# Optimization experiments

Hardware: AMD Instinct MI355X
Metric: run time of the kernel (lower is better)

## Reference

```python
import jax, jax.numpy as jnp
import numpy as np

N_NODES = 100000
N_EDGES = 1600000
IN_NODE = 129
HID = 128
N_LAYERS = 3


def setup_inputs() -> dict:
    key = jax.random.key(0)
    ks = jax.random.split(key, 20)
    gnn_in = IN_NODE - 1
    x = jax.random.normal(ks[0], (N_NODES, IN_NODE), dtype=jnp.float32)
    edge_index = jax.random.randint(ks[1], (2, N_EDGES), 0, N_NODES, dtype=jnp.int64)
    edge_attr = jax.random.uniform(ks[2], (N_EDGES, 1), dtype=jnp.float32)
    # conv layer params: lin (in->hid) per layer, scalar edge mlp per layer
    dims = [gnn_in] + [HID] * N_LAYERS
    conv_W, conv_b, edge_w = [], [], []
    for i in range(N_LAYERS):
        fin = dims[i]
        s = 1.0 / np.sqrt(fin)
        conv_W.append(jax.random.uniform(ks[3 + i], (fin, HID), jnp.float32, -s, s))
        conv_b.append(jax.random.uniform(ks[6 + i], (HID,), jnp.float32, -s, s))
        edge_w.append(jax.random.uniform(ks[9 + i], (1, 1), jnp.float32, -1.0, 1.0))
    h2 = HID // 2
    t_h = IN_NODE // 2
    s1 = 1.0 / np.sqrt(HID + 1)
    s2 = 1.0 / np.sqrt(h2)
    s3 = 1.0 / np.sqrt(IN_NODE)
    s4 = 1.0 / np.sqrt(t_h)
    return {
        "x": x, "edge_index": edge_index, "edge_attr": edge_attr,
        "conv_W": tuple(conv_W), "conv_b": tuple(conv_b), "edge_w": tuple(edge_w),
        "lin1_W": jax.random.uniform(ks[12], (HID + 1, h2), jnp.float32, -s1, s1),
        "lin1_b": jax.random.uniform(ks[13], (h2,), jnp.float32, -s1, s1),
        "lin2_W": jax.random.uniform(ks[14], (h2, 1), jnp.float32, -s2, s2),
        "lin2_b": jax.random.uniform(ks[15], (1,), jnp.float32, -s2, s2),
        "t1_W": jax.random.uniform(ks[16], (IN_NODE, t_h), jnp.float32, -s3, s3),
        "t1_b": jax.random.uniform(ks[17], (t_h,), jnp.float32, -s3, s3),
        "t2_W": jax.random.uniform(ks[18], (t_h, 1), jnp.float32, -s4, s4),
        "t2_b": jax.random.uniform(ks[19], (1,), jnp.float32, -s4, s4),
    }


def reference(x, edge_index, edge_attr, conv_W, conv_b, edge_w,
              lin1_W, lin1_b, lin2_W, lin2_b, t1_W, t1_b, t2_W, t2_b):
    n = x.shape[0]
    # add self loops with edge_attr fill_value = 1.0
    loops = jnp.arange(n, dtype=edge_index.dtype)
    src = jnp.concatenate([edge_index[0], loops])
    tgt = jnp.concatenate([edge_index[1], loops])
    ea = jnp.concatenate([edge_attr, jnp.ones((n, 1), edge_attr.dtype)], axis=0)  # [E+N,1]
    # in-degree for mean aggregation (>=1 because of self loops)
    deg = jax.ops.segment_sum(jnp.ones_like(ea[:, 0]), tgt, num_segments=n)[:, None]
    # treatment head (eval mode: no dropout)
    t = jax.nn.relu(x @ t1_W + t1_b)
    t = jax.nn.sigmoid(t @ t2_W + t2_b)  # [N,1]
    h = x[:, 1:]
    for W, b, w in zip(conv_W, conv_b, edge_w):
        ht = h @ W + b                          # [N,HID]
        gate = jax.nn.sigmoid(ea * w[0, 0])     # [E+N,1]
        msg = gate * ht[src]                    # gather + gate
        agg = jax.ops.segment_sum(msg, tgt, num_segments=n) / deg
        h = jax.nn.relu(agg)
    z = jnp.concatenate([h, t], axis=1)          # [N,HID+1]
    z = jax.nn.relu(z @ lin1_W + lin1_b)
    out = jax.nn.sigmoid(z @ lin2_W + lin2_b)[:, 0]  # [N]
    return out
```

## Files before the change

kernel.cpp:

```cpp
#include <hip/hip_runtime.h>
#include <hip/hip_fp16.h>
#include <math.h>


typedef _Float16 f16x8 __attribute__((ext_vector_type(8)));
typedef float f32x4 __attribute__((ext_vector_type(4)));

#define EPB 1024

__device__ __forceinline__ float sigmoidf_(float v) { return 1.f / (1.f + expf(-v)); }

__global__ void sentinel_kernel(float* __restrict__ out, int n, float val) {
  int i = blockIdx.x * 256 + threadIdx.x;
  if (i < n) out[i] = val;
}

__global__ void flag_kernel(const int* __restrict__ ei, int* __restrict__ flag) {
  if (threadIdx.x == 0 && blockIdx.x == 0) {
    int all0 = 1;
    for (int k = 1; k < 512; k += 2) {
      if (ei[k] != 0) { all0 = 0; break; }
    }
    *flag = all0;
  }
}

__global__ __launch_bounds__(256) void hist_kernel(const int* __restrict__ ei,
    int E, int n, const int* __restrict__ flag, int* __restrict__ histA,
    int nblocksA, int NB) {
  __shared__ int hl[512];
  for (int i = threadIdx.x; i < NB; i += 256) hl[i] = 0;
  __syncthreads();
  int f64 = *flag;
  const long long* e64 = (const long long*)ei;
  int base = blockIdx.x * EPB;
  int end = min(base + EPB, E);
  for (int e = base + threadIdx.x; e < end; e += 256) {
    int t = f64 ? (int)e64[(size_t)E + e] : ei[(size_t)E + e];
    if ((unsigned)t < (unsigned)n) atomicAdd(&hl[t >> 8], 1);
  }
  __syncthreads();
  for (int i = threadIdx.x; i < NB; i += 256)
    histA[(size_t)i * nblocksA + blockIdx.x] = hl[i];
}

__global__ __launch_bounds__(256) void scanrow_kernel(int* __restrict__ histA,
    int nblocksA, int* __restrict__ binTotal) {
  __shared__ int tmp[256];
  int bin = blockIdx.x;
  int* row = histA + (size_t)bin * nblocksA;
  int carry = 0;
  for (int c0 = 0; c0 < nblocksA; c0 += 256) {
    int i = c0 + threadIdx.x;
    int v = (i < nblocksA) ? row[i] : 0;
    tmp[threadIdx.x] = v;
    __syncthreads();
    for (int off = 1; off < 256; off <<= 1) {
      int t = (threadIdx.x >= (unsigned)off) ? tmp[threadIdx.x - off] : 0;
      __syncthreads();
      tmp[threadIdx.x] += t;
      __syncthreads();
    }
    if (i < nblocksA) row[i] = carry + tmp[threadIdx.x] - v;
    carry += tmp[255];
    __syncthreads();
  }
  if (threadIdx.x == 0) binTotal[bin] = carry;
}

__global__ void binbase_kernel(const int* __restrict__ binTotal, int NB,
                               int* __restrict__ binBase, int* __restrict__ starts,
                               int n) {
  __shared__ int tmp[512];
  int v = (threadIdx.x < (unsigned)NB) ? binTotal[threadIdx.x] : 0;
  tmp[threadIdx.x] = v;
  __syncthreads();
  for (int off = 1; off < 512; off <<= 1) {
    int t = (threadIdx.x >= (unsigned)off) ? tmp[threadIdx.x - off] : 0;
    __syncthreads();
    tmp[threadIdx.x] += t;
    __syncthreads();
  }
  if (threadIdx.x < (unsigned)NB) binBase[threadIdx.x] = tmp[threadIdx.x] - v;
  if (threadIdx.x == (unsigned)(NB - 1)) {
    binBase[NB] = tmp[threadIdx.x];
    starts[n] = tmp[threadIdx.x];
  }
}

__global__ __launch_bounds__(256) void reorder_kernel(const int* __restrict__ ei,
    const float* __restrict__ ea, int E, int n, const int* __restrict__ flag,
    const int* __restrict__ histA, int nblocksA, const int* __restrict__ binBase,
    const float* __restrict__ w0p, const float* __restrict__ w1p,
    const float* __restrict__ w2p, uint2* __restrict__ brec,
    unsigned char* __restrict__ bkey, int NB) {
  __shared__ int cur[512];
  for (int i = threadIdx.x; i < NB; i += 256)
    cur[i] = binBase[i] + histA[(size_t)i * nblocksA + blockIdx.x];
  __syncthreads();
  float w0 = w0p[0], w1 = w1p[0], w2 = w2p[0];
  int f64 = *flag;
  const long long* e64 = (const long long*)ei;
  int base = blockIdx.x * EPB;
  int end = min(base + EPB, E);
  for (int e = base + threadIdx.x; e < end; e += 256) {
    int s, t;
    if (f64) { s = (int)e64[e]; t = (int)e64[(size_t)E + e]; }
    else     { s = ei[e];       t = ei[(size_t)E + e]; }
    if ((unsigned)t < (unsigned)n) {
      int pos = atomicAdd(&cur[t >> 8], 1);
      float a = ea[e];
      unsigned sn = (unsigned)min(max(s, 0), min(n - 1, 0x1ffff));
      unsigned g0 = (unsigned)__float2uint_rn(sigmoidf_(a * w0) * 32767.f);
      unsigned g1 = (unsigned)__float2uint_rn(sigmoidf_(a * w1) * 32767.f);
      unsigned g2 = (unsigned)__float2uint_rn(sigmoidf_(a * w2) * 32767.f);
      brec[pos] = make_uint2(sn | (g0 << 17), g1 | (g2 << 15));
      bkey[pos] = (unsigned char)(t & 255);
    }
  }
}

__global__ __launch_bounds__(256) void fine_kernel(const uint2* __restrict__ brec,
    const unsigned char* __restrict__ bkey, const int* __restrict__ binBase,
    int n, uint2* __restrict__ csr, int* __restrict__ starts) {
  __shared__ int cnt[256];
  __shared__ int offs[256];
  __shared__ int tmp[256];
  int bin = blockIdx.x;
  int b0 = binBase[bin], b1 = binBase[bin + 1];
  cnt[threadIdx.x] = 0;
  __syncthreads();
  for (int p = b0 + threadIdx.x; p < b1; p += 256)
    atomicAdd(&cnt[bkey[p]], 1);
  __syncthreads();
  int v = cnt[threadIdx.x];
  tmp[threadIdx.x] = v;
  __syncthreads();
  for (int off = 1; off < 256; off <<= 1) {
    int t = (threadIdx.x >= (unsigned)off) ? tmp[threadIdx.x - off] : 0;
    __syncthreads();
    tmp[threadIdx.x] += t;
    __syncthreads();
  }
  offs[threadIdx.x] = tmp[threadIdx.x] - v;
  int node = bin * 256 + threadIdx.x;
  if (node < n) starts[node] = b0 + offs[threadIdx.x];
  __syncthreads();
  cnt[threadIdx.x] = 0;
  __syncthreads();
  for (int p = b0 + threadIdx.x; p < b1; p += 256) {
    int k = bkey[p];
    int l = atomicAdd(&cnt[k], 1);
    csr[b0 + offs[k] + l] = brec[p];
  }
}

__global__ void slice_kernel(const float* __restrict__ x, _Float16* __restrict__ h,
                             float* __restrict__ x0, int n) {
  int idx = blockIdx.x * blockDim.x + threadIdx.x;
  if (idx < n * 128) {
    int node = idx >> 7;
    int k = idx & 127;
    h[idx] = (_Float16)x[(size_t)node * 129 + 1 + k];
  }
  if (idx < n) x0[idx] = x[(size_t)idx * 129];
}

__global__ __launch_bounds__(256) void head_mfma_kernel(const _Float16* __restrict__ h,
    const float* __restrict__ extra, const float* __restrict__ W1,
    const float* __restrict__ b1, const float* __restrict__ w2,
    const float* __restrict__ b2, float* __restrict__ out, int n,
    int hrow0, int xrow) {
  __shared__ __align__(16) _Float16 sB[4 * 4 * 64 * 8];
  __shared__ float sWx[64], sB1[64], sW2[64];
  for (int idx = threadIdx.x; idx < 8192; idx += 256) {
    int k = idx >> 6, col = idx & 63;
    float w = W1[(size_t)(hrow0 + k) * 64 + col];
    int ks = k >> 5, quad = (k >> 3) & 3, j = k & 7;
    int nt = col >> 4, cl = col & 15;
    sB[(((ks * 4 + nt) * 64) + quad * 16 + cl) * 8 + j] = (_Float16)w;
  }
  if (threadIdx.x < 64) {
    sWx[threadIdx.x] = W1[(size_t)xrow * 64 + threadIdx.x];
    sB1[threadIdx.x] = b1[threadIdx.x];
    sW2[threadIdx.x] = w2[threadIdx.x];
  }
  __syncthreads();
  int wv = threadIdx.x >> 6, lane = threadIdx.x & 63;
  int quad = lane >> 4, l15 = lane & 15;
  int n0 = (blockIdx.x * 4 + wv) * 16;
  if (n0 >= n) return;
  int node_a = min(n0 + l15, n - 1);
  const _Float16* hrow = h + (size_t)node_a * 128 + quad * 8;

  f32x4 acc[4];
#pragma unroll
  for (int t = 0; t < 4; t++) acc[t] = (f32x4){0.f, 0.f, 0.f, 0.f};
  for (int ks = 0; ks < 4; ks++) {
    f16x8 afrag = *(const f16x8*)(hrow + ks * 32);
    const f16x8* bp = (const f16x8*)sB;
#pragma unroll
    for (int t = 0; t < 4; t++) {
      f16x8 bfrag = bp[(ks * 4 + t) * 64 + lane];
      acc[t] = __builtin_amdgcn_mfma_f32_16x16x32_f16(afrag, bfrag, acc[t], 0, 0, 0);
    }
  }
  float b2v = b2[0];
  float xv[4], part[4] = {0.f, 0.f, 0.f, 0.f};
#pragma unroll
  for (int r = 0; r < 4; r++) xv[r] = extra[min(n0 + quad * 4 + r, n - 1)];
#pragma unroll
  for (int t = 0; t < 4; t++) {
    int col = t * 16 + l15;
    float wx = sWx[col], bb = sB1[col], w2v = sW2[col];
#pragma unroll
    for (int r = 0; r < 4; r++) {
      float u = fmaxf(acc[t][r] + xv[r] * wx + bb, 0.f);
      part[r] += u * w2v;
    }
  }
#pragma unroll
  for (int r = 0; r < 4; r++) {
    float p = part[r];
    p += __shfl_xor(p, 1); p += __shfl_xor(p, 2);
    p += __shfl_xor(p, 4); p += __shfl_xor(p, 8);
    int node = n0 + quad * 4 + r;
    if (l15 == 0 && node < n) out[node] = sigmoidf_(p + b2v);
  }
}

__global__ __launch_bounds__(256) void gemm_mfma_kernel(const _Float16* __restrict__ h,
    const float* __restrict__ Wg, const float* __restrict__ b,
    unsigned char* __restrict__ out8, float* __restrict__ scales, int n) {
  __shared__ __align__(16) _Float16 sB[4 * 8 * 64 * 8];
  for (int i = threadIdx.x; i < 4096; i += 256) {
    int k = i >> 5;
    int n4 = (i & 31) * 4;
    float4 w4 = ((const float4*)Wg)[i];
    int ks = k >> 5, quad = (k >> 3) & 3, j = k & 7;
#pragma unroll
    for (int c = 0; c < 4; c++) {
      int col = n4 + c;
      int nt = col >> 4, cl = col & 15;
      sB[(((ks * 8 + nt) * 64) + quad * 16 + cl) * 8 + j] =
          (_Float16)((const float*)&w4)[c];
    }
  }
  __syncthreads();
  int wv = threadIdx.x >> 6, lane = threadIdx.x & 63;
  int quad = lane >> 4, l15 = lane & 15;
  int tiles = (n + 63) >> 6;
  for (int tile = blockIdx.x; tile < tiles; tile += gridDim.x) {
    int n0 = (tile * 4 + wv) * 16;
    if (n0 >= n) continue;
    int node_a = min(n0 + l15, n - 1);
    const _Float16* hrow = h + (size_t)node_a * 128 + quad * 8;

    f32x4 acc[8];
#pragma unroll
    for (int t = 0; t < 8; t++) acc[t] = (f32x4){0.f, 0.f, 0.f, 0.f};

    for (int ks = 0; ks < 4; ks++) {
      f16x8 afrag = *(const f16x8*)(hrow + ks * 32);
      const f16x8* bp = (const f16x8*)(sB + ks * 8 * 64 * 8);
#pragma unroll
      for (int t = 0; t < 8; t++) {
        f16x8 bfrag = bp[t * 64 + lane];
        acc[t] = __builtin_amdgcn_mfma_f32_16x16x32_f16(afrag, bfrag, acc[t], 0, 0, 0);
      }
    }
#pragma unroll
    for (int t = 0; t < 8; t++) {
      float bias = b[t * 16 + l15];
#pragma unroll
      for (int r = 0; r < 4; r++) acc[t][r] += bias;
    }
    float mx[4] = {0.f, 0.f, 0.f, 0.f};
#pragma unroll
    for (int t = 0; t < 8; t++)
#pragma unroll
      for (int r = 0; r < 4; r++) mx[r] = fmaxf(mx[r], fabsf(acc[t][r]));
#pragma unroll
    for (int m = 1; m <= 8; m <<= 1) {
#pragma unroll
      for (int r = 0; r < 4; r++) mx[r] = fmaxf(mx[r], __shfl_xor(mx[r], m));
    }
#pragma unroll
    for (int r = 0; r < 4; r++) {
      int node = n0 + quad * 4 + r;
      if (node >= n) continue;
      float inv = (mx[r] > 0.f) ? 127.f / mx[r] : 0.f;
      if (l15 == 0) scales[node] = mx[r] * (1.f / 127.f);
#pragma unroll
      for (int t = 0; t < 8; t++) {
        int u = (int)rintf(acc[t][r] * inv) + 128;
        u = min(max(u, 0), 255);
        out8[(size_t)node * 128 + t * 16 + l15] = (unsigned char)u;
      }
    }
  }
}

template <int LAYER>
__device__ __forceinline__ float gate_(uint2 r) {
  const float inv = 1.f / 32767.f;
  if (LAYER == 0) return (float)(r.x >> 17) * inv;
  if (LAYER == 1) return (float)(r.y & 0x7fffu) * inv;
  return (float)(r.y >> 15) * inv;
}

#define ACC4(u, g)                                   \
  a0 += (float)((u) & 0xffu) * (g);                  \
  a1 += (float)(((u) >> 8) & 0xffu) * (g);           \
  a2 += (float)(((u) >> 16) & 0xffu) * (g);          \
  a3 += (float)((u) >> 24) * (g);

template <int LAYER>
__global__ __launch_bounds__(256) void agg_kernel(const unsigned char* __restrict__ ht8,
    const float* __restrict__ scales, const uint2* __restrict__ csr,
    const int* __restrict__ starts, const float* __restrict__ wp,
    __half2* __restrict__ hout, int n) {
  int wv = threadIdx.x >> 6, lane = threadIdx.x & 63;
  int node = blockIdx.x * 4 + wv;
  if (node >= n) return;
  int s = starts[node];
  int c = starts[node + 1] - s;
  float gs = sigmoidf_(wp[0]);
  int sub = lane & 31, p = lane >> 5;
  unsigned sub4 = (unsigned)sub * 4u;

  unsigned su = *(const unsigned*)(ht8 + (unsigned)node * 128u + sub4);
  float gsc = (p == 0) ? gs * scales[node] : 0.f;
  float sgs = gsc;
  float a0 = 0.f, a1 = 0.f, a2 = 0.f, a3 = 0.f;
  ACC4(su, gsc)

  int j = 0;
  for (; j + 16 <= c; j += 16) {
    uint2 r0 = csr[s + j + 0 + p],  r1 = csr[s + j + 2 + p];
    uint2 r2 = csr[s + j + 4 + p],  r3 = csr[s + j + 6 + p];
    uint2 r4 = csr[s + j + 8 + p],  r5 = csr[s + j + 10 + p];
    uint2 r6 = csr[s + j + 12 + p], r7 = csr[s + j + 14 + p];
    unsigned i0 = r0.x & 0x1ffffu, i1 = r1.x & 0x1ffffu;
    unsigned i2 = r2.x & 0x1ffffu, i3 = r3.x & 0x1ffffu;
    unsigned i4 = r4.x & 0x1ffffu, i5 = r5.x & 0x1ffffu;
    unsigned i6 = r6.x & 0x1ffffu, i7 = r7.x & 0x1ffffu;
    unsigned u0 = *(const unsigned*)(ht8 + i0 * 128u + sub4);
    unsigned u1 = *(const unsigned*)(ht8 + i1 * 128u + sub4);
    unsigned u2 = *(const unsigned*)(ht8 + i2 * 128u + sub4);
    unsigned u3 = *(const unsigned*)(ht8 + i3 * 128u + sub4);
    unsigned u4 = *(const unsigned*)(ht8 + i4 * 128u + sub4);
    unsigned u5 = *(const unsigned*)(ht8 + i5 * 128u + sub4);
    unsigned u6 = *(const unsigned*)(ht8 + i6 * 128u + sub4);
    unsigned u7 = *(const unsigned*)(ht8 + i7 * 128u + sub4);
    float g0 = gate_<LAYER>(r0) * scales[i0];
    float g1 = gate_<LAYER>(r1) * scales[i1];
    float g2 = gate_<LAYER>(r2) * scales[i2];
    float g3 = gate_<LAYER>(r3) * scales[i3];
    float g4 = gate_<LAYER>(r4) * scales[i4];
    float g5 = gate_<LAYER>(r5) * scales[i5];
    float g6 = gate_<LAYER>(r6) * scales[i6];
    float g7 = gate_<LAYER>(r7) * scales[i7];
    sgs += g0 + g1 + g2 + g3 + g4 + g5 + g6 + g7;
    ACC4(u0, g0) ACC4(u1, g1) ACC4(u2, g2) ACC4(u3, g3)
    ACC4(u4, g4) ACC4(u5, g5) ACC4(u6, g6) ACC4(u7, g7)
  }
  for (; j + 8 <= c; j += 8) {
    uint2 r0 = csr[s + j + 0 + p], r1 = csr[s + j + 2 + p];
    uint2 r2 = csr[s + j + 4 + p], r3 = csr[s + j + 6 + p];
    unsigned i0 = r0.x & 0x1ffffu, i1 = r1.x & 0x1ffffu;
    unsigned i2 = r2.x & 0x1ffffu, i3 = r3.x & 0x1ffffu;
    unsigned u0 = *(const unsigned*)(ht8 + i0 * 128u + sub4);
    unsigned u1 = *(const unsigned*)(ht8 + i1 * 128u + sub4);
    unsigned u2 = *(const unsigned*)(ht8 + i2 * 128u + sub4);
    unsigned u3 = *(const unsigned*)(ht8 + i3 * 128u + sub4);
    float g0 = gate_<LAYER>(r0) * scales[i0];
    float g1 = gate_<LAYER>(r1) * scales[i1];
    float g2 = gate_<LAYER>(r2) * scales[i2];
    float g3 = gate_<LAYER>(r3) * scales[i3];
    sgs += g0 + g1 + g2 + g3;
    ACC4(u0, g0) ACC4(u1, g1) ACC4(u2, g2) ACC4(u3, g3)
  }
  for (; j + 2 <= c; j += 2) {
    uint2 r = csr[s + j + p];
    unsigned i0 = r.x & 0x1ffffu;
    unsigned u = *(const unsigned*)(ht8 + i0 * 128u + sub4);
    float g = gate_<LAYER>(r) * scales[i0];
    sgs += g;
    ACC4(u, g)
  }
  if (j < c) {
    uint2 r = csr[s + j];
    unsigned i0 = r.x & 0x1ffffu;
    unsigned u = *(const unsigned*)(ht8 + i0 * 128u + sub4);
    float g = (p == 0) ? gate_<LAYER>(r) * scales[i0] : 0.f;
    sgs += g;
    ACC4(u, g)
  }
  a0 += __shfl_xor(a0, 32); a1 += __shfl_xor(a1, 32);
  a2 += __shfl_xor(a2, 32); a3 += __shfl_xor(a3, 32);
  sgs += __shfl_xor(sgs, 32);
  float corr = 128.f * sgs;
  float inv = 1.f / (float)(c + 1);
  a0 = fmaxf((a0 - corr) * inv, 0.f);
  a1 = fmaxf((a1 - corr) * inv, 0.f);
  a2 = fmaxf((a2 - corr) * inv, 0.f);
  a3 = fmaxf((a3 - corr) * inv, 0.f);
  if (p == 0) {
    __half2 h01 = __floats2half2_rn(a0, a1);
    __half2 h23 = __floats2half2_rn(a2, a3);
    uint2 outw;
    outw.x = *(unsigned*)&h01;
    outw.y = *(unsigned*)&h23;
    *(uint2*)((char*)hout + (size_t)node * 256 + (size_t)sub * 8) = outw;
  }
}

extern "C" void kernel_launch(void* const* d_in, const int* in_sizes, int n_in,
                              void* d_out, int out_size, void* d_ws, size_t ws_size,
                              hipStream_t stream) {
  int ob = (out_size + 255) / 256;

  const float *x, *ea, *l1W, *l1b, *l2W, *l2b, *t1W, *t1b, *t2W, *t2b;
  const float *convW[3], *convb[3], *edgew[3];
  const int* ei;

  if (n_in == 20) {
    x = (const float*)d_in[0]; ei = (const int*)d_in[1]; ea = (const float*)d_in[2];
    for (int l = 0; l < 3; l++) {
      convW[l] = (const float*)d_in[3 + l];
      convb[l] = (const float*)d_in[6 + l];
      edgew[l] = (const float*)d_in[9 + l];
    }
    l1W = (const float*)d_in[12]; l1b = (const float*)d_in[13];
    l2W = (const float*)d_in[14]; l2b = (const float*)d_in[15];
    t1W = (const float*)d_in[16]; t1b = (const float*)d_in[17];
    t2W = (const float*)d_in[18]; t2b = (const float*)d_in[19];
  } else if (n_in == 14) {
    x = (const float*)d_in[0]; ei = (const int*)d_in[1]; ea = (const float*)d_in[2];
    const float* cw = (const float*)d_in[3];
    const float* cb = (const float*)d_in[4];
    const float* ew = (const float*)d_in[5];
    for (int l = 0; l < 3; l++) {
      convW[l] = cw + (size_t)l * 128 * 128;
      convb[l] = cb + (size_t)l * 128;
      edgew[l] = ew + l;
    }
    l1W = (const float*)d_in[6];  l1b = (const float*)d_in[7];
    l2W = (const float*)d_in[8];  l2b = (const float*)d_in[9];
    t1W = (const float*)d_in[10]; t1b = (const float*)d_in[11];
    t2W = (const float*)d_in[12]; t2b = (const float*)d_in[13];
  } else {
    sentinel_kernel<<<ob, 256, 0, stream>>>((float*)d_out, out_size,
                                            900.0f + (float)n_in);
    return;
  }

  int n = in_sizes[0] / 129;
  int E = in_sizes[2];

  int nblocksA = (E + EPB - 1) / EPB;
  int NB = (n + 255) >> 8;

  char* ws = (char*)d_ws;
  size_t off = 0;
  auto take = [&](size_t bytes) -> void* {
    void* p = ws + off;
    off = (off + bytes + 255) & ~(size_t)255;
    return p;
  };
  int*      flag    = (int*)take(256);
  int*      histA   = (int*)take((size_t)NB * nblocksA * 4);
  int*      binTot  = (int*)take((size_t)NB * 4);
  int*      binBase = (int*)take(((size_t)NB + 1) * 4);
  int*      starts  = (int*)take(((size_t)n + 1) * 4);
  uint2*    brec    = (uint2*)take((size_t)E * 8);
  unsigned char* bkey = (unsigned char*)take((size_t)E);
  uint2*    csr     = (uint2*)take((size_t)E * 8);
  float*    tbuf    = (float*)take((size_t)n * 4);
  float*    x0buf   = (float*)take((size_t)n * 4);
  _Float16* h16     = (_Float16*)take((size_t)n * 128 * 2);
  unsigned char* ht8 = (unsigned char*)take((size_t)n * 128);
  float*    scales  = (float*)take((size_t)n * 4);

  if (off > ws_size || nblocksA > 4096 || NB > 512) {
    sentinel_kernel<<<ob, 256, 0, stream>>>((float*)d_out, out_size,
                                            1000.0f + (float)(ws_size >> 20));
    return;
  }

  int sb = (int)(((size_t)n * 128 + 255) / 256);
  int hgrid = (n + 63) / 64;

  flag_kernel<<<1, 64, 0, stream>>>(ei, flag);
  hist_kernel<<<nblocksA, 256, 0, stream>>>(ei, E, n, flag, histA, nblocksA, NB);
  scanrow_kernel<<<NB, 256, 0, stream>>>(histA, nblocksA, binTot);
  binbase_kernel<<<1, 512, 0, stream>>>(binTot, NB, binBase, starts, n);
  reorder_kernel<<<nblocksA, 256, 0, stream>>>(ei, ea, E, n, flag, histA, nblocksA,
                                               binBase, edgew[0], edgew[1], edgew[2],
                                               brec, bkey, NB);
  fine_kernel<<<NB, 256, 0, stream>>>(brec, bkey, binBase, n, csr, starts);

  slice_kernel<<<sb, 256, 0, stream>>>(x, h16, x0buf, n);
  head_mfma_kernel<<<hgrid, 256, 0, stream>>>(h16, x0buf, t1W, t1b, t2W, t2b,
                                              tbuf, n, 1, 0);

  int gemm_grid = min((n + 63) / 64, 1024);
  gemm_mfma_kernel<<<gemm_grid, 256, 0, stream>>>(h16, convW[0], convb[0], ht8, scales, n);
  agg_kernel<0><<<(n + 3) / 4, 256, 0, stream>>>(ht8, scales, csr, starts,
                                                 edgew[0], (__half2*)h16, n);
  gemm_mfma_kernel<<<gemm_grid, 256, 0, stream>>>(h16, convW[1], convb[1], ht8, scales, n);
  agg_kernel<1><<<(n + 3) / 4, 256, 0, stream>>>(ht8, scales, csr, starts,
                                                 edgew[1], (__half2*)h16, n);
  gemm_mfma_kernel<<<gemm_grid, 256, 0, stream>>>(h16, convW[2], convb[2], ht8, scales, n);
  agg_kernel<2><<<(n + 3) / 4, 256, 0, stream>>>(ht8, scales, csr, starts,
                                                 edgew[2], (__half2*)h16, n);

  head_mfma_kernel<<<hgrid, 256, 0, stream>>>(h16, tbuf, l1W, l1b, l2W, l2b,
                                              (float*)d_out, n, 0, 128);
}
```

Measured before the change: 476.3 us.

## Split fine CSR bucketing into four sub-blocks per bin with quarter histograms

The per-bin fine sort now runs as two kernels. The first builds a 256-key histogram for each quarter of a bin. The second uses the summed quarters to compute each quarter's write offsets and scatters its slice independently. With NB around 391 bins, this raises the grid from one block per bin to four, which should improve GPU occupancy on a serial-heavy phase. In exchange it adds a kernel launch, a small qhist buffer, and a second pass reading bkey.

```diff
diff --git a/kernel.cpp b/kernel.cpp
--- a/kernel.cpp
+++ b/kernel.cpp
@@ -120,20 +120,35 @@
   }
 }
 
-__global__ __launch_bounds__(256) void fine_kernel(const uint2* __restrict__ brec,
+__global__ __launch_bounds__(256) void fineA_kernel(const unsigned char* __restrict__ bkey,
+    const int* __restrict__ binBase, int* __restrict__ qhist) {
+  __shared__ int cnt[256];
+  int bin = blockIdx.x >> 2, q = blockIdx.x & 3;
+  int b0 = binBase[bin], b1 = binBase[bin + 1];
+  int len = b1 - b0;
+  int q0 = b0 + (len * q) / 4, q1 = b0 + (len * (q + 1)) / 4;
+  cnt[threadIdx.x] = 0;
+  __syncthreads();
+  for (int p = q0 + threadIdx.x; p < q1; p += 256)
+    atomicAdd(&cnt[bkey[p]], 1);
+  __syncthreads();
+  qhist[((size_t)bin * 4 + q) * 256 + threadIdx.x] = cnt[threadIdx.x];
+}
+
+__global__ __launch_bounds__(256) void fineB_kernel(const uint2* __restrict__ brec,
     const unsigned char* __restrict__ bkey, const int* __restrict__ binBase,
-    int n, uint2* __restrict__ csr, int* __restrict__ starts) {
-  __shared__ int cnt[256];
-  __shared__ int offs[256];
+    const int* __restrict__ qhist, int n, uint2* __restrict__ csr,
+    int* __restrict__ starts) {
+  __shared__ int cur[256];
   __shared__ int tmp[256];
-  int bin = blockIdx.x;
+  int bin = blockIdx.x >> 2, q = blockIdx.x & 3;
   int b0 = binBase[bin], b1 = binBase[bin + 1];
-  cnt[threadIdx.x] = 0;
-  __syncthreads();
-  for (int p = b0 + threadIdx.x; p < b1; p += 256)
-    atomicAdd(&cnt[bkey[p]], 1);
-  __syncthreads();
-  int v = cnt[threadIdx.x];
+  int len = b1 - b0;
+  int q0 = b0 + (len * q) / 4, q1 = b0 + (len * (q + 1)) / 4;
+  const int* qh = qhist + (size_t)bin * 4 * 256;
+  int c0 = qh[threadIdx.x], c1 = qh[256 + threadIdx.x];
+  int c2 = qh[512 + threadIdx.x], c3 = qh[768 + threadIdx.x];
+  int v = c0 + c1 + c2 + c3;
   tmp[threadIdx.x] = v;
   __syncthreads();
   for (int off = 1; off < 256; off <<= 1) {
@@ -142,16 +157,16 @@
     tmp[threadIdx.x] += t;
     __syncthreads();
   }
-  offs[threadIdx.x] = tmp[threadIdx.x] - v;
+  int offk = tmp[threadIdx.x] - v;
+  int base_q = (q > 0 ? c0 : 0) + (q > 1 ? c1 : 0) + (q > 2 ? c2 : 0);
+  cur[threadIdx.x] = b0 + offk + base_q;
   int node = bin * 256 + threadIdx.x;
-  if (node < n) starts[node] = b0 + offs[threadIdx.x];
-  __syncthreads();
-  cnt[threadIdx.x] = 0;
-  __syncthreads();
-  for (int p = b0 + threadIdx.x; p < b1; p += 256) {
+  if (q == 0 && node < n) starts[node] = b0 + offk;
+  __syncthreads();
+  for (int p = q0 + threadIdx.x; p < q1; p += 256) {
     int k = bkey[p];
-    int l = atomicAdd(&cnt[k], 1);
-    csr[b0 + offs[k] + l] = brec[p];
+    int l = atomicAdd(&cur[k], 1);
+    csr[l] = brec[p];
   }
 }
 
@@ -473,6 +488,7 @@
   int*      histA   = (int*)take((size_t)NB * nblocksA * 4);
   int*      binTot  = (int*)take((size_t)NB * 4);
   int*      binBase = (int*)take(((size_t)NB + 1) * 4);
+  int*      qhist   = (int*)take((size_t)NB * 4 * 256 * 4);
   int*      starts  = (int*)take(((size_t)n + 1) * 4);
   uint2*    brec    = (uint2*)take((size_t)E * 8);
   unsigned char* bkey = (unsigned char*)take((size_t)E);
@@ -499,7 +515,8 @@
   reorder_kernel<<<nblocksA, 256, 0, stream>>>(ei, ea, E, n, flag, histA, nblocksA,
                                                binBase, edgew[0], edgew[1], edgew[2],
                                                brec, bkey, NB);
-  fine_kernel<<<NB, 256, 0, stream>>>(brec, bkey, binBase, n, csr, starts);
+  fineA_kernel<<<NB * 4, 256, 0, stream>>>(bkey, binBase, qhist);
+  fineB_kernel<<<NB * 4, 256, 0, stream>>>(brec, bkey, binBase, qhist, n, csr, starts);
 
   slice_kernel<<<sb, 256, 0, stream>>>(x, h16, x0buf, n);
   head_mfma_kernel<<<hgrid, 256, 0, stream>>>(h16, x0buf, t1W, t1b, t2W, t2b,
```

New measurement: 477.7 us. About the same (+0.3%).
